# Performance work log

Hardware: AMD Instinct MI355X
Metric: run time of the kernel (lower is better)

Reference implementation:

```python
import jax, jax.numpy as jnp
import numpy as np

B, N, D, L = 32, 1024, 128, 2  # batch graphs, nodes, hidden dim, num GIN layers
BN_EPS = 1e-5


def _batchnorm(x2d, gamma, beta):
    # Training-mode BatchNorm1d over flattened (B*N, D) with biased variance
    mean = jnp.mean(x2d, axis=0)
    var = jnp.mean(jnp.square(x2d - mean), axis=0)
    return (x2d - mean) * (gamma / jnp.sqrt(var + BN_EPS)) + beta


def setup_inputs() -> dict:
    key = jax.random.key(0)
    ks = jax.random.split(key, 12)
    s = 1.0 / np.sqrt(D)  # torch Linear default init scale
    inp = {
        "x": jax.random.normal(ks[0], (B, N, D), dtype=jnp.float32),
        "padded_nei": jax.random.randint(ks[1], (B, N, 8), 0, N, dtype=jnp.int64),
        "adj": jax.random.uniform(ks[2], (B, N, N), dtype=jnp.float32),
        # stacked per-layer params [L, ...]
        "W1": jax.random.uniform(ks[3], (L, D, D), jnp.float32, -s, s),
        "b1": jax.random.uniform(ks[4], (L, D), jnp.float32, -s, s),
        "W2": jax.random.uniform(ks[5], (L, D, D), jnp.float32, -s, s),
        "b2": jax.random.uniform(ks[6], (L, D), jnp.float32, -s, s),
        "g_in": jnp.ones((L, D), jnp.float32),   # MLP-internal BN gamma
        "be_in": jnp.zeros((L, D), jnp.float32),  # MLP-internal BN beta
        "g_out": jnp.ones((L, D), jnp.float32),  # GraphCNN outer BN gamma
        "be_out": jnp.zeros((L, D), jnp.float32),
    }
    return inp


def reference(x, padded_nei, adj, W1, b1, W2, b2, g_in, be_in, g_out, be_out):
    h = x  # [B, N, D]
    for l in range(L):
        # sum-pooling over neighbors via batched dense adjacency matmul
        pooled = jnp.einsum('bij,bjd->bid', adj, h)  # [B, N, D]
        # MLP: Linear -> BN -> ReLU -> Linear
        z = pooled @ W1[l] + b1[l]
        z = jax.nn.relu(_batchnorm(z.reshape(-1, D), g_in[l], be_in[l])).reshape(B, N, D)
        z = z @ W2[l] + b2[l]
        # outer BatchNorm1d + ReLU
        h = jax.nn.relu(_batchnorm(z.reshape(-1, D), g_out[l], be_out[l])).reshape(B, N, D)
    return h
```

## Files before the change

### kernel.cpp

```cpp
#include <hip/hip_runtime.h>
#include <stdint.h>


#define BB 32
#define NN 1024
#define DD 128
#define RR 32768

typedef __bf16 bf16_t;
typedef bf16_t bf16x8 __attribute__((ext_vector_type(8)));
typedef float f32x4 __attribute__((ext_vector_type(4)));

__device__ __forceinline__ unsigned short f2b(float f) {
  unsigned u = __float_as_uint(f);
  u += 0x7fff + ((u >> 16) & 1);
  return (unsigned short)(u >> 16);
}
__device__ __forceinline__ float b2f(unsigned short s) {
  return __uint_as_float((unsigned)s << 16);
}

#define GLL(GP, LP)                                              \
  __builtin_amdgcn_global_load_lds(                              \
      (const __attribute__((address_space(1))) void*)(GP),       \
      (__attribute__((address_space(3))) void*)(LP), 16, 0, 0)

__global__ __launch_bounds__(256) void k0_prep(const float* __restrict__ x,
                                               const float* __restrict__ W1,
                                               const float* __restrict__ W2,
                                               unsigned short* __restrict__ hT,
                                               unsigned short* __restrict__ W1T,
                                               unsigned short* __restrict__ W2T) {
  const int tid = threadIdx.x;
  if (blockIdx.x < 256) {
    const int b = blockIdx.x >> 3, nt = blockIdx.x & 7;
    __shared__ alignas(16) unsigned short T[128][136];
    const int r = tid >> 1, c0 = (tid & 1) * 64;
    const float* src = x + ((size_t)(b * 8 + nt) * 128 + r) * 128 + c0;
#pragma unroll
    for (int i = 0; i < 64; i += 4) {
      float4 v = *(const float4*)(src + i);
      int c = c0 + i;
      T[c][r] = f2b(v.x); T[c + 1][r] = f2b(v.y);
      T[c + 2][r] = f2b(v.z); T[c + 3][r] = f2b(v.w);
    }
    __syncthreads();
    const int d = tid >> 1, n0 = (tid & 1) * 64;
    unsigned short* dst = hT + ((size_t)b * DD + d) * NN + nt * 128 + n0;
#pragma unroll
    for (int i = 0; i < 64; i += 8)
      *(uint4*)(dst + i) = *(const uint4*)&T[d][n0 + i];
  } else {
    int idx = (blockIdx.x - 256) * 256 + tid;
    int w = idx >> 15;
    int rem = idx & 32767;
    int l = rem >> 14;
    int n = (rem >> 7) & 127;
    int k = rem & 127;
    const float* W = w ? W2 : W1;
    unsigned short* WT = w ? W2T : W1T;
    WT[((size_t)l * 128 + n) * 128 + k] = f2b(W[((size_t)l * 128 + k) * 128 + n]);
  }
}

__global__ __launch_bounds__(256, 2) void kA_pool_lin(
    const float* __restrict__ adj, const unsigned short* __restrict__ hT,
    const unsigned short* __restrict__ WT, const float* __restrict__ bias,
    unsigned short* __restrict__ z1b, float* __restrict__ gsum,
    float* __restrict__ gsq) {
  const int mt = blockIdx.x, b = blockIdx.y;
  const int tid = threadIdx.x;
  const int wave = tid >> 6, lane = tid & 63;
  const int wc = wave * 32;
  const int ln = lane & 15, q = lane >> 4;

  __shared__ union {
    struct {
      float A[2][4096];
      unsigned short Bst[2][8192];
    } s;
    unsigned short As2[64][136];
  } sm;

  bf16x8 wfr[4][2];
#pragma unroll
  for (int ks = 0; ks < 4; ks++)
#pragma unroll
    for (int j = 0; j < 2; j++)
      wfr[ks][j] = *(const bf16x8*)&WT[(size_t)(wc + j * 16 + ln) * 128 + ks * 32 + q * 8];
  asm volatile("s_waitcnt vmcnt(0)" ::: "memory");

  const int rA = tid >> 4, uA = tid & 15;
  const float* gAf = adj + ((size_t)b * NN + mt * 64 + rA) * NN + ((uA ^ (rA & 7)) << 2);
  const int rB = tid >> 3, uB = tid & 7;
  const unsigned short* gBs =
      hT + (size_t)b * DD * NN + (size_t)rB * NN + ((uB ^ (rB & 7)) << 3);

#define STAGE(P, K0)                                \
  do {                                              \
    float* ap = sm.s.A[(P)];                        \
    unsigned short* bp = sm.s.Bst[(P)];             \
    GLL(gAf + (K0), ap + tid * 4);                  \
    GLL(gAf + 16 * NN + (K0), ap + 1024 + tid * 4); \
    GLL(gAf + 32 * NN + (K0), ap + 2048 + tid * 4); \
    GLL(gAf + 48 * NN + (K0), ap + 3072 + tid * 4); \
    GLL(gBs + (K0), bp + tid * 8);                  \
    GLL(gBs + 32 * NN + (K0), bp + 2048 + tid * 8); \
    GLL(gBs + 64 * NN + (K0), bp + 4096 + tid * 8); \
    GLL(gBs + 96 * NN + (K0), bp + 6144 + tid * 8); \
  } while (0)

  STAGE(0, 0);
  STAGE(1, 64);

  f32x4 acc1[4][2];
  f32x4 zero = {0.f, 0.f, 0.f, 0.f};
#pragma unroll
  for (int i = 0; i < 4; i++) { acc1[i][0] = zero; acc1[i][1] = zero; }

  const int x7 = ln & 7;
  const int xorvB = x7 << 4;

#pragma unroll 2
  for (int t = 0; t < 16; ++t) {
    const int p = t & 1;
    if (t < 15)
      asm volatile("s_waitcnt vmcnt(8)" ::: "memory");
    else
      asm volatile("s_waitcnt vmcnt(0)" ::: "memory");
    __builtin_amdgcn_s_barrier();
    __builtin_amdgcn_sched_barrier(0);
    {
      const float* Ab = sm.s.A[p];
      const char* Bb = (const char*)sm.s.Bst[p];
#pragma unroll
      for (int kk = 0; kk < 2; kk++) {
        const int cu = kk * 8 + q * 2;
        bf16x8 af[4], bfr[2];
#pragma unroll
        for (int i = 0; i < 4; i++) {
          const float* arow = Ab + (i * 16 + ln) * 64;
          float4 a0 = *(const float4*)(arow + ((cu ^ x7) << 2));
          float4 a1 = *(const float4*)(arow + (((cu + 1) ^ x7) << 2));
          bf16x8 v;
          v[0] = (bf16_t)a0.x; v[1] = (bf16_t)a0.y;
          v[2] = (bf16_t)a0.z; v[3] = (bf16_t)a0.w;
          v[4] = (bf16_t)a1.x; v[5] = (bf16_t)a1.y;
          v[6] = (bf16_t)a1.z; v[7] = (bf16_t)a1.w;
          af[i] = v;
        }
#pragma unroll
        for (int j = 0; j < 2; j++)
          bfr[j] = *(const bf16x8*)(Bb + (wc + j * 16 + ln) * 128 +
                                    (((kk << 6) + (q << 4)) ^ xorvB));
#pragma unroll
        for (int i = 0; i < 4; i++)
#pragma unroll
          for (int j = 0; j < 2; j++)
            acc1[i][j] = __builtin_amdgcn_mfma_f32_16x16x32_bf16(af[i], bfr[j], acc1[i][j], 0, 0, 0);
      }
    }
    __builtin_amdgcn_sched_barrier(0);
    __builtin_amdgcn_s_barrier();
    __builtin_amdgcn_sched_barrier(0);
    if (t < 14) STAGE(p, (t + 2) * 64);
  }
#undef STAGE

#pragma unroll
  for (int i = 0; i < 4; i++) {
    int row = i * 16 + q * 4;
#pragma unroll
    for (int j = 0; j < 2; j++) {
      int col = wc + j * 16 + ln;
#pragma unroll
      for (int r = 0; r < 4; r++) sm.As2[row + r][col] = f2b(acc1[i][j][r]);
    }
  }
  __syncthreads();

  f32x4 acc2[4][2];
#pragma unroll
  for (int i = 0; i < 4; i++) { acc2[i][0] = zero; acc2[i][1] = zero; }
#pragma unroll
  for (int ks = 0; ks < 4; ks++) {
    bf16x8 af[4];
#pragma unroll
    for (int i = 0; i < 4; i++)
      af[i] = *(const bf16x8*)&sm.As2[i * 16 + ln][ks * 32 + q * 8];
#pragma unroll
    for (int i = 0; i < 4; i++)
#pragma unroll
      for (int j = 0; j < 2; j++)
        acc2[i][j] = __builtin_amdgcn_mfma_f32_16x16x32_bf16(af[i], wfr[ks][j], acc2[i][j], 0, 0, 0);
  }

  const size_t row0 = (size_t)b * NN + mt * 64;
#pragma unroll
  for (int j = 0; j < 2; j++) {
    int col = wc + j * 16 + ln;
    float bc = bias[col];
    float s1 = 0.f, s2 = 0.f;
#pragma unroll
    for (int i = 0; i < 4; i++) {
      int row = i * 16 + q * 4;
#pragma unroll
      for (int r = 0; r < 4; r++) {
        float v = acc2[i][j][r] + bc;
        z1b[(row0 + row + r) * 128 + col] = f2b(v);
        s1 += v; s2 += v * v;
      }
    }
    s1 += __shfl_xor(s1, 16); s1 += __shfl_xor(s1, 32);
    s2 += __shfl_xor(s2, 16); s2 += __shfl_xor(s2, 32);
    if (q == 0) { atomicAdd(&gsum[col], s1); atomicAdd(&gsq[col], s2); }
  }
}

__global__ __launch_bounds__(256, 2) void kB_lin(
    const unsigned short* __restrict__ Zin, const float* __restrict__ gsum_in,
    const float* __restrict__ gsq_in, const float* __restrict__ gamma,
    const float* __restrict__ beta, const unsigned short* __restrict__ WT,
    const float* __restrict__ bias, unsigned short* __restrict__ z2b,
    float* __restrict__ gsum, float* __restrict__ gsq) {
  const int mt = blockIdx.x;
  const int tid = threadIdx.x;
  const int wave = tid >> 6, lane = tid & 63;
  const int wc = wave * 32;
  const int ln = lane & 15, q = lane >> 4;

  __shared__ alignas(16) unsigned short Az[64][136];
  __shared__ alignas(16) unsigned short Ws[128][136];
  __shared__ float nsc[128], nsh[128];

  if (tid < 128) {
    float mean = gsum_in[tid] * (1.f / 32768.f);
    float var = gsq_in[tid] * (1.f / 32768.f) - mean * mean;
    float sc = gamma[tid] * rsqrtf(var + 1e-5f);
    nsc[tid] = sc; nsh[tid] = beta[tid] - mean * sc;
  }
#pragma unroll
  for (int p = 0; p < 8; p++) {
    int c = tid + p * 256;
    int n = c >> 4, k8 = (c & 15) * 8;
    *(uint4*)&Ws[n][k8] = *(const uint4*)&WT[n * 128 + k8];
  }
  __syncthreads();

  const size_t row0 = (size_t)mt * 64;
  {
    const int r = tid >> 2, c0 = (tid & 3) * 32;
    const unsigned short* src = Zin + (row0 + r) * 128 + c0;
#pragma unroll
    for (int u = 0; u < 4; u++) {
      uint4 raw = *(const uint4*)(src + u * 8);
      const unsigned short* s = (const unsigned short*)&raw;
      alignas(16) unsigned short t[8];
#pragma unroll
      for (int e = 0; e < 8; e++) {
        int c = c0 + u * 8 + e;
        t[e] = f2b(fmaxf(fmaf(b2f(s[e]), nsc[c], nsh[c]), 0.f));
      }
      *(uint4*)&Az[r][c0 + u * 8] = *(const uint4*)&t[0];
    }
  }
  __syncthreads();

  f32x4 acc[4][2];
  f32x4 zero = {0.f, 0.f, 0.f, 0.f};
#pragma unroll
  for (int i = 0; i < 4; i++) { acc[i][0] = zero; acc[i][1] = zero; }
#pragma unroll
  for (int ks = 0; ks < 4; ks++) {
    bf16x8 af[4], bfr[2];
#pragma unroll
    for (int i = 0; i < 4; i++)
      af[i] = *(const bf16x8*)&Az[i * 16 + ln][ks * 32 + q * 8];
#pragma unroll
    for (int j = 0; j < 2; j++)
      bfr[j] = *(const bf16x8*)&Ws[wc + j * 16 + ln][ks * 32 + q * 8];
#pragma unroll
    for (int i = 0; i < 4; i++)
#pragma unroll
      for (int j = 0; j < 2; j++)
        acc[i][j] = __builtin_amdgcn_mfma_f32_16x16x32_bf16(af[i], bfr[j], acc[i][j], 0, 0, 0);
  }

#pragma unroll
  for (int j = 0; j < 2; j++) {
    int col = wc + j * 16 + ln;
    float bc = bias[col];
    float s1 = 0.f, s2 = 0.f;
#pragma unroll
    for (int i = 0; i < 4; i++) {
      int row = i * 16 + q * 4;
#pragma unroll
      for (int r = 0; r < 4; r++) {
        float v = acc[i][j][r] + bc;
        z2b[(row0 + row + r) * 128 + col] = f2b(v);
        s1 += v; s2 += v * v;
      }
    }
    s1 += __shfl_xor(s1, 16); s1 += __shfl_xor(s1, 32);
    s2 += __shfl_xor(s2, 16); s2 += __shfl_xor(s2, 32);
    if (q == 0) { atomicAdd(&gsum[col], s1); atomicAdd(&gsq[col], s2); }
  }
}

__global__ __launch_bounds__(256) void k4_bnt(const unsigned short* __restrict__ Z,
                                              const float* __restrict__ gsum,
                                              const float* __restrict__ gsq,
                                              const float* __restrict__ gamma,
                                              const float* __restrict__ beta,
                                              unsigned short* __restrict__ hT) {
  const int b = blockIdx.x, nt = blockIdx.y, tid = threadIdx.x;
  __shared__ alignas(16) unsigned short T[128][136];
  __shared__ float nsc[128], nsh[128];
  if (tid < 128) {
    float mean = gsum[tid] * (1.f / 32768.f);
    float var = gsq[tid] * (1.f / 32768.f) - mean * mean;
    float sc = gamma[tid] * rsqrtf(var + 1e-5f);
    nsc[tid] = sc; nsh[tid] = beta[tid] - mean * sc;
  }
  __syncthreads();
  const int r = tid >> 1, c0 = (tid & 1) * 64;
  const unsigned short* src = Z + ((size_t)(b * 8 + nt) * 128 + r) * 128 + c0;
#pragma unroll
  for (int u = 0; u < 8; u++) {
    uint4 raw = *(const uint4*)(src + u * 8);
    const unsigned short* s = (const unsigned short*)&raw;
#pragma unroll
    for (int e = 0; e < 8; e++) {
      int c = c0 + u * 8 + e;
      T[c][r] = f2b(fmaxf(fmaf(b2f(s[e]), nsc[c], nsh[c]), 0.f));
    }
  }
  __syncthreads();
  const int d = tid >> 1, n0 = (tid & 1) * 64;
  unsigned short* dst = hT + ((size_t)b * DD + d) * NN + nt * 128 + n0;
#pragma unroll
  for (int i = 0; i < 64; i += 8)
    *(uint4*)(dst + i) = *(const uint4*)&T[d][n0 + i];
}

__global__ __launch_bounds__(256) void k4_out(const unsigned short* __restrict__ Z,
                                              const float* __restrict__ gsum,
                                              const float* __restrict__ gsq,
                                              const float* __restrict__ gamma,
                                              const float* __restrict__ beta,
                                              float* __restrict__ out) {
  const int blk = blockIdx.x, tid = threadIdx.x;
  __shared__ float nsc[128], nsh[128];
  if (tid < 128) {
    float mean = gsum[tid] * (1.f / 32768.f);
    float var = gsq[tid] * (1.f / 32768.f) - mean * mean;
    float sc = gamma[tid] * rsqrtf(var + 1e-5f);
    nsc[tid] = sc; nsh[tid] = beta[tid] - mean * sc;
  }
  __syncthreads();
  const int r = tid >> 1, c0 = (tid & 1) * 64;
  const unsigned short* src = Z + ((size_t)blk * 128 + r) * 128 + c0;
  float* dst = out + ((size_t)blk * 128 + r) * 128 + c0;
#pragma unroll
  for (int u = 0; u < 8; u++) {
    uint4 raw = *(const uint4*)(src + u * 8);
    const unsigned short* s = (const unsigned short*)&raw;
    float4 o;
    int c = c0 + u * 8;
    o.x = fmaxf(fmaf(b2f(s[0]), nsc[c], nsh[c]), 0.f);
    o.y = fmaxf(fmaf(b2f(s[1]), nsc[c + 1], nsh[c + 1]), 0.f);
    o.z = fmaxf(fmaf(b2f(s[2]), nsc[c + 2], nsh[c + 2]), 0.f);
    o.w = fmaxf(fmaf(b2f(s[3]), nsc[c + 3], nsh[c + 3]), 0.f);
    *(float4*)(dst + u * 8) = o;
    o.x = fmaxf(fmaf(b2f(s[4]), nsc[c + 4], nsh[c + 4]), 0.f);
    o.y = fmaxf(fmaf(b2f(s[5]), nsc[c + 5], nsh[c + 5]), 0.f);
    o.z = fmaxf(fmaf(b2f(s[6]), nsc[c + 6], nsh[c + 6]), 0.f);
    o.w = fmaxf(fmaf(b2f(s[7]), nsc[c + 7], nsh[c + 7]), 0.f);
    *(float4*)(dst + u * 8 + 4) = o;
  }
}

extern "C" void kernel_launch(void* const* d_in, const int* in_sizes, int n_in,
                              void* d_out, int out_size, void* d_ws, size_t ws_size,
                              hipStream_t stream) {
  const float* x = (const float*)d_in[0];
  const float* adj = (const float*)d_in[2];
  const float* W1 = (const float*)d_in[3];
  const float* b1 = (const float*)d_in[4];
  const float* W2 = (const float*)d_in[5];
  const float* b2 = (const float*)d_in[6];
  const float* g_in = (const float*)d_in[7];
  const float* be_in = (const float*)d_in[8];
  const float* g_out = (const float*)d_in[9];
  const float* be_out = (const float*)d_in[10];
  float* out = (float*)d_out;

  char* ws = (char*)d_ws;
  unsigned short* hT = (unsigned short*)ws;
  unsigned short* z1b = (unsigned short*)(ws + 8ull * 1024 * 1024);
  unsigned short* z2b = (unsigned short*)(ws + 16ull * 1024 * 1024);
  unsigned short* W1T = (unsigned short*)(ws + 24ull * 1024 * 1024);
  unsigned short* W2T = W1T + 2 * 128 * 128;
  float* stats = (float*)(ws + 25ull * 1024 * 1024);

  hipMemsetAsync(stats, 0, 4 * 256 * sizeof(float), stream);
  k0_prep<<<512, 256, 0, stream>>>(x, W1, W2, hT, W1T, W2T);

  for (int l = 0; l < 2; l++) {
    float* st_in = stats + (l * 2 + 0) * 256;
    float* st_out = stats + (l * 2 + 1) * 256;
    kA_pool_lin<<<dim3(16, 32), 256, 0, stream>>>(adj, hT, W1T + l * 16384,
                                                  b1 + l * 128, z1b, st_in,
                                                  st_in + 128);
    kB_lin<<<512, 256, 0, stream>>>(z1b, st_in, st_in + 128, g_in + l * 128,
                                    be_in + l * 128, W2T + l * 16384,
                                    b2 + l * 128, z2b, st_out, st_out + 128);
    if (l == 0)
      k4_bnt<<<dim3(32, 8), 256, 0, stream>>>(z2b, st_out, st_out + 128, g_out,
                                              be_out, hT);
    else
      k4_out<<<256, 256, 0, stream>>>(z2b, st_out, st_out + 128, g_out + 128,
                                      be_out + 128, out);
  }
}
```

Before: 344.7 us.

## Fuse all stages into one persistent kernel with grid-wide barriers

Replaces the sequence of prep, pool+linear, linear, and BN-transpose/output launches with a single 512-block kernel that separates phases using a software grid barrier (atomic counter plus generation flag). The aim is to remove per-launch overhead and the idle tail between dependent kernels. It relies on all 512 blocks being co-resident (two per CU at 256 threads), and barrier spinning plus fences add their own latency. Shared memory becomes a union sized for the largest phase.

```diff
diff --git a/kernel.cpp b/kernel.cpp
--- a/kernel.cpp
+++ b/kernel.cpp
@@ -6,6 +6,7 @@
 #define NN 1024
 #define DD 128
 #define RR 32768
+#define NBLK 512
 
 typedef __bf16 bf16_t;
 typedef bf16_t bf16x8 __attribute__((ext_vector_type(8)));
@@ -25,33 +26,76 @@
       (const __attribute__((address_space(1))) void*)(GP),       \
       (__attribute__((address_space(3))) void*)(LP), 16, 0, 0)
 
-__global__ __launch_bounds__(256) void k0_prep(const float* __restrict__ x,
-                                               const float* __restrict__ W1,
-                                               const float* __restrict__ W2,
-                                               unsigned short* __restrict__ hT,
-                                               unsigned short* __restrict__ W1T,
-                                               unsigned short* __restrict__ W2T) {
+__device__ __forceinline__ void gsync(unsigned* bar) {
+  __syncthreads();
+  if (threadIdx.x == 0) {
+    __threadfence();
+    unsigned gen = __hip_atomic_load(bar + 1, __ATOMIC_RELAXED,
+                                     __HIP_MEMORY_SCOPE_AGENT);
+    unsigned prev = __hip_atomic_fetch_add(bar, 1u, __ATOMIC_ACQ_REL,
+                                           __HIP_MEMORY_SCOPE_AGENT);
+    if (prev == (unsigned)(NBLK - 1)) {
+      __hip_atomic_store(bar, 0u, __ATOMIC_RELAXED, __HIP_MEMORY_SCOPE_AGENT);
+      __hip_atomic_fetch_add(bar + 1, 1u, __ATOMIC_RELEASE,
+                             __HIP_MEMORY_SCOPE_AGENT);
+    } else {
+      while (__hip_atomic_load(bar + 1, __ATOMIC_RELAXED,
+                               __HIP_MEMORY_SCOPE_AGENT) == gen)
+        __builtin_amdgcn_s_sleep(2);
+    }
+    __threadfence();
+  }
+  __syncthreads();
+}
+
+__global__ __launch_bounds__(256, 2) void k_all(
+    const float* __restrict__ x, const float* __restrict__ adj,
+    const float* __restrict__ W1, const float* __restrict__ b1,
+    const float* __restrict__ W2, const float* __restrict__ b2,
+    const float* __restrict__ g_in, const float* __restrict__ be_in,
+    const float* __restrict__ g_out, const float* __restrict__ be_out,
+    float* __restrict__ out, unsigned short* __restrict__ hT,
+    unsigned short* __restrict__ z1b, unsigned short* __restrict__ z2b,
+    unsigned short* __restrict__ W1T, unsigned short* __restrict__ W2T,
+    float* __restrict__ stats, unsigned* __restrict__ bar) {
+  const int blk = blockIdx.x;
   const int tid = threadIdx.x;
-  if (blockIdx.x < 256) {
-    const int b = blockIdx.x >> 3, nt = blockIdx.x & 7;
-    __shared__ alignas(16) unsigned short T[128][136];
+
+  __shared__ union {
+    struct {
+      alignas(16) unsigned short T[128][136];
+    } t;
+    struct {
+      float A[2][4096];
+      unsigned short Bst[2][8192];
+    } a;
+    unsigned short As2[64][136];
+    struct {
+      alignas(16) unsigned short Az[64][136];
+      alignas(16) unsigned short Ws[128][136];
+    } b;
+  } sm;
+  __shared__ float nsc[128], nsh[128];
+
+  if (blk < 256) {
+    const int b = blk >> 3, nt = blk & 7;
     const int r = tid >> 1, c0 = (tid & 1) * 64;
     const float* src = x + ((size_t)(b * 8 + nt) * 128 + r) * 128 + c0;
 #pragma unroll
     for (int i = 0; i < 64; i += 4) {
       float4 v = *(const float4*)(src + i);
       int c = c0 + i;
-      T[c][r] = f2b(v.x); T[c + 1][r] = f2b(v.y);
-      T[c + 2][r] = f2b(v.z); T[c + 3][r] = f2b(v.w);
+      sm.t.T[c][r] = f2b(v.x); sm.t.T[c + 1][r] = f2b(v.y);
+      sm.t.T[c + 2][r] = f2b(v.z); sm.t.T[c + 3][r] = f2b(v.w);
     }
     __syncthreads();
     const int d = tid >> 1, n0 = (tid & 1) * 64;
     unsigned short* dst = hT + ((size_t)b * DD + d) * NN + nt * 128 + n0;
 #pragma unroll
     for (int i = 0; i < 64; i += 8)
-      *(uint4*)(dst + i) = *(const uint4*)&T[d][n0 + i];
+      *(uint4*)(dst + i) = *(const uint4*)&sm.t.T[d][n0 + i];
   } else {
-    int idx = (blockIdx.x - 256) * 256 + tid;
+    int idx = (blk - 256) * 256 + tid;
     int w = idx >> 15;
     int rem = idx & 32767;
     int l = rem >> 14;
@@ -61,322 +105,302 @@
     unsigned short* WT = w ? W2T : W1T;
     WT[((size_t)l * 128 + n) * 128 + k] = f2b(W[((size_t)l * 128 + k) * 128 + n]);
   }
-}
-
-__global__ __launch_bounds__(256, 2) void kA_pool_lin(
-    const float* __restrict__ adj, const unsigned short* __restrict__ hT,
-    const unsigned short* __restrict__ WT, const float* __restrict__ bias,
-    unsigned short* __restrict__ z1b, float* __restrict__ gsum,
-    float* __restrict__ gsq) {
-  const int mt = blockIdx.x, b = blockIdx.y;
-  const int tid = threadIdx.x;
-  const int wave = tid >> 6, lane = tid & 63;
-  const int wc = wave * 32;
-  const int ln = lane & 15, q = lane >> 4;
-
-  __shared__ union {
-    struct {
-      float A[2][4096];
-      unsigned short Bst[2][8192];
-    } s;
-    unsigned short As2[64][136];
-  } sm;
-
-  bf16x8 wfr[4][2];
-#pragma unroll
-  for (int ks = 0; ks < 4; ks++)
-#pragma unroll
-    for (int j = 0; j < 2; j++)
-      wfr[ks][j] = *(const bf16x8*)&WT[(size_t)(wc + j * 16 + ln) * 128 + ks * 32 + q * 8];
-  asm volatile("s_waitcnt vmcnt(0)" ::: "memory");
-
-  const int rA = tid >> 4, uA = tid & 15;
-  const float* gAf = adj + ((size_t)b * NN + mt * 64 + rA) * NN + ((uA ^ (rA & 7)) << 2);
-  const int rB = tid >> 3, uB = tid & 7;
-  const unsigned short* gBs =
-      hT + (size_t)b * DD * NN + (size_t)rB * NN + ((uB ^ (rB & 7)) << 3);
-
-#define STAGE(P, K0)                                \
-  do {                                              \
-    float* ap = sm.s.A[(P)];                        \
-    unsigned short* bp = sm.s.Bst[(P)];             \
-    GLL(gAf + (K0), ap + tid * 4);                  \
-    GLL(gAf + 16 * NN + (K0), ap + 1024 + tid * 4); \
-    GLL(gAf + 32 * NN + (K0), ap + 2048 + tid * 4); \
-    GLL(gAf + 48 * NN + (K0), ap + 3072 + tid * 4); \
-    GLL(gBs + (K0), bp + tid * 8);                  \
-    GLL(gBs + 32 * NN + (K0), bp + 2048 + tid * 8); \
-    GLL(gBs + 64 * NN + (K0), bp + 4096 + tid * 8); \
-    GLL(gBs + 96 * NN + (K0), bp + 6144 + tid * 8); \
+  gsync(bar);
+
+  for (int l = 0; l < 2; ++l) {
+    float* st_in = stats + (l * 2 + 0) * 256;
+    float* st_out = stats + (l * 2 + 1) * 256;
+
+    {
+      const int mt = blk & 15, b = blk >> 4;
+      const int wave = tid >> 6, lane = tid & 63;
+      const int wc = wave * 32;
+      const int ln = lane & 15, q = lane >> 4;
+      const unsigned short* WTa = W1T + l * 16384;
+      const float* biasA = b1 + l * 128;
+
+      bf16x8 wfr[4][2];
+#pragma unroll
+      for (int ks = 0; ks < 4; ks++)
+#pragma unroll
+        for (int j = 0; j < 2; j++)
+          wfr[ks][j] = *(const bf16x8*)&WTa[(size_t)(wc + j * 16 + ln) * 128 + ks * 32 + q * 8];
+      asm volatile("s_waitcnt vmcnt(0)" ::: "memory");
+
+      const int rA = tid >> 4, uA = tid & 15;
+      const float* gAf = adj + ((size_t)b * NN + mt * 64 + rA) * NN + ((uA ^ (rA & 7)) << 2);
+      const int rB = tid >> 3, uB = tid & 7;
+      const unsigned short* gBs =
+          hT + (size_t)b * DD * NN + (size_t)rB * NN + ((uB ^ (rB & 7)) << 3);
+
+#define STAGE(P, K0)                                  \
+  do {                                                \
+    float* ap = sm.a.A[(P)];                          \
+    unsigned short* bp = sm.a.Bst[(P)];               \
+    GLL(gAf + (K0), ap + tid * 4);                    \
+    GLL(gAf + 16 * NN + (K0), ap + 1024 + tid * 4);   \
+    GLL(gAf + 32 * NN + (K0), ap + 2048 + tid * 4);   \
+    GLL(gAf + 48 * NN + (K0), ap + 3072 + tid * 4);   \
+    GLL(gBs + (K0), bp + tid * 8);                    \
+    GLL(gBs + 32 * NN + (K0), bp + 2048 + tid * 8);   \
+    GLL(gBs + 64 * NN + (K0), bp + 4096 + tid * 8);   \
+    GLL(gBs + 96 * NN + (K0), bp + 6144 + tid * 8);   \
   } while (0)
 
-  STAGE(0, 0);
-  STAGE(1, 64);
-
-  f32x4 acc1[4][2];
-  f32x4 zero = {0.f, 0.f, 0.f, 0.f};
-#pragma unroll
-  for (int i = 0; i < 4; i++) { acc1[i][0] = zero; acc1[i][1] = zero; }
-
-  const int x7 = ln & 7;
-  const int xorvB = x7 << 4;
+      STAGE(0, 0);
+      STAGE(1, 64);
+
+      f32x4 acc1[4][2];
+      f32x4 zero = {0.f, 0.f, 0.f, 0.f};
+#pragma unroll
+      for (int i = 0; i < 4; i++) { acc1[i][0] = zero; acc1[i][1] = zero; }
+
+      const int x7 = ln & 7;
+      const int xorvB = x7 << 4;
 
 #pragma unroll 2
-  for (int t = 0; t < 16; ++t) {
-    const int p = t & 1;
-    if (t < 15)
-      asm volatile("s_waitcnt vmcnt(8)" ::: "memory");
-    else
-      asm volatile("s_waitcnt vmcnt(0)" ::: "memory");
-    __builtin_amdgcn_s_barrier();
-    __builtin_amdgcn_sched_barrier(0);
+      for (int t = 0; t < 16; ++t) {
+        const int p = t & 1;
+        if (t < 15)
+          asm volatile("s_waitcnt vmcnt(8)" ::: "memory");
+        else
+          asm volatile("s_waitcnt vmcnt(0)" ::: "memory");
+        __builtin_amdgcn_s_barrier();
+        __builtin_amdgcn_sched_barrier(0);
+        {
+          const float* Ab = sm.a.A[p];
+          const char* Bb = (const char*)sm.a.Bst[p];
+#pragma unroll
+          for (int kk = 0; kk < 2; kk++) {
+            const int cu = kk * 8 + q * 2;
+            bf16x8 af[4], bfr[2];
+#pragma unroll
+            for (int i = 0; i < 4; i++) {
+              const float* arow = Ab + (i * 16 + ln) * 64;
+              float4 a0 = *(const float4*)(arow + ((cu ^ x7) << 2));
+              float4 a1 = *(const float4*)(arow + (((cu + 1) ^ x7) << 2));
+              bf16x8 v;
+              v[0] = (bf16_t)a0.x; v[1] = (bf16_t)a0.y;
+              v[2] = (bf16_t)a0.z; v[3] = (bf16_t)a0.w;
+              v[4] = (bf16_t)a1.x; v[5] = (bf16_t)a1.y;
+              v[6] = (bf16_t)a1.z; v[7] = (bf16_t)a1.w;
+              af[i] = v;
+            }
+#pragma unroll
+            for (int j = 0; j < 2; j++)
+              bfr[j] = *(const bf16x8*)(Bb + (wc + j * 16 + ln) * 128 +
+                                        (((kk << 6) + (q << 4)) ^ xorvB));
+#pragma unroll
+            for (int i = 0; i < 4; i++)
+#pragma unroll
+              for (int j = 0; j < 2; j++)
+                acc1[i][j] = __builtin_amdgcn_mfma_f32_16x16x32_bf16(af[i], bfr[j], acc1[i][j], 0, 0, 0);
+          }
+        }
+        __builtin_amdgcn_sched_barrier(0);
+        __builtin_amdgcn_s_barrier();
+        __builtin_amdgcn_sched_barrier(0);
+        if (t < 14) STAGE(p, (t + 2) * 64);
+      }
+#undef STAGE
+
+#pragma unroll
+      for (int i = 0; i < 4; i++) {
+        int row = i * 16 + q * 4;
+#pragma unroll
+        for (int j = 0; j < 2; j++) {
+          int col = wc + j * 16 + ln;
+#pragma unroll
+          for (int r = 0; r < 4; r++) sm.As2[row + r][col] = f2b(acc1[i][j][r]);
+        }
+      }
+      __syncthreads();
+
+      f32x4 acc2[4][2];
+#pragma unroll
+      for (int i = 0; i < 4; i++) { acc2[i][0] = zero; acc2[i][1] = zero; }
+#pragma unroll
+      for (int ks = 0; ks < 4; ks++) {
+        bf16x8 af[4];
+#pragma unroll
+        for (int i = 0; i < 4; i++)
+          af[i] = *(const bf16x8*)&sm.As2[i * 16 + ln][ks * 32 + q * 8];
+#pragma unroll
+        for (int i = 0; i < 4; i++)
+#pragma unroll
+          for (int j = 0; j < 2; j++)
+            acc2[i][j] = __builtin_amdgcn_mfma_f32_16x16x32_bf16(af[i], wfr[ks][j], acc2[i][j], 0, 0, 0);
+      }
+
+      const size_t row0 = (size_t)b * NN + mt * 64;
+#pragma unroll
+      for (int j = 0; j < 2; j++) {
+        int col = wc + j * 16 + ln;
+        float bc = biasA[col];
+        float s1 = 0.f, s2 = 0.f;
+#pragma unroll
+        for (int i = 0; i < 4; i++) {
+          int row = i * 16 + q * 4;
+#pragma unroll
+          for (int r = 0; r < 4; r++) {
+            float v = acc2[i][j][r] + bc;
+            z1b[(row0 + row + r) * 128 + col] = f2b(v);
+            s1 += v; s2 += v * v;
+          }
+        }
+        s1 += __shfl_xor(s1, 16); s1 += __shfl_xor(s1, 32);
+        s2 += __shfl_xor(s2, 16); s2 += __shfl_xor(s2, 32);
+        if (q == 0) { atomicAdd(&st_in[col], s1); atomicAdd(&st_in[128 + col], s2); }
+      }
+    }
+    gsync(bar);
+
     {
-      const float* Ab = sm.s.A[p];
-      const char* Bb = (const char*)sm.s.Bst[p];
-#pragma unroll
-      for (int kk = 0; kk < 2; kk++) {
-        const int cu = kk * 8 + q * 2;
+      const int mt = blk;
+      const int wave = tid >> 6, lane = tid & 63;
+      const int wc = wave * 32;
+      const int ln = lane & 15, q = lane >> 4;
+      const unsigned short* WTb = W2T + l * 16384;
+      const float* biasB = b2 + l * 128;
+      const float* gam = g_in + l * 128;
+      const float* bet = be_in + l * 128;
+
+      if (tid < 128) {
+        float mean = st_in[tid] * (1.f / 32768.f);
+        float var = st_in[128 + tid] * (1.f / 32768.f) - mean * mean;
+        float sc = gam[tid] * rsqrtf(var + 1e-5f);
+        nsc[tid] = sc; nsh[tid] = bet[tid] - mean * sc;
+      }
+#pragma unroll
+      for (int p = 0; p < 8; p++) {
+        int c = tid + p * 256;
+        int n = c >> 4, k8 = (c & 15) * 8;
+        *(uint4*)&sm.b.Ws[n][k8] = *(const uint4*)&WTb[n * 128 + k8];
+      }
+      __syncthreads();
+
+      const size_t row0 = (size_t)mt * 64;
+      {
+        const int r = tid >> 2, c0 = (tid & 3) * 32;
+        const unsigned short* src = z1b + (row0 + r) * 128 + c0;
+#pragma unroll
+        for (int u = 0; u < 4; u++) {
+          uint4 raw = *(const uint4*)(src + u * 8);
+          const unsigned short* s = (const unsigned short*)&raw;
+          alignas(16) unsigned short tmp[8];
+#pragma unroll
+          for (int e = 0; e < 8; e++) {
+            int c = c0 + u * 8 + e;
+            tmp[e] = f2b(fmaxf(fmaf(b2f(s[e]), nsc[c], nsh[c]), 0.f));
+          }
+          *(uint4*)&sm.b.Az[r][c0 + u * 8] = *(const uint4*)&tmp[0];
+        }
+      }
+      __syncthreads();
+
+      f32x4 acc[4][2];
+      f32x4 zero = {0.f, 0.f, 0.f, 0.f};
+#pragma unroll
+      for (int i = 0; i < 4; i++) { acc[i][0] = zero; acc[i][1] = zero; }
+#pragma unroll
+      for (int ks = 0; ks < 4; ks++) {
         bf16x8 af[4], bfr[2];
 #pragma unroll
+        for (int i = 0; i < 4; i++)
+          af[i] = *(const bf16x8*)&sm.b.Az[i * 16 + ln][ks * 32 + q * 8];
+#pragma unroll
+        for (int j = 0; j < 2; j++)
+          bfr[j] = *(const bf16x8*)&sm.b.Ws[wc + j * 16 + ln][ks * 32 + q * 8];
+#pragma unroll
+        for (int i = 0; i < 4; i++)
+#pragma unroll
+          for (int j = 0; j < 2; j++)
+            acc[i][j] = __builtin_amdgcn_mfma_f32_16x16x32_bf16(af[i], bfr[j], acc[i][j], 0, 0, 0);
+      }
+
+#pragma unroll
+      for (int j = 0; j < 2; j++) {
+        int col = wc + j * 16 + ln;
+        float bc = biasB[col];
+        float s1 = 0.f, s2 = 0.f;
+#pragma unroll
         for (int i = 0; i < 4; i++) {
-          const float* arow = Ab + (i * 16 + ln) * 64;
-          float4 a0 = *(const float4*)(arow + ((cu ^ x7) << 2));
-          float4 a1 = *(const float4*)(arow + (((cu + 1) ^ x7) << 2));
-          bf16x8 v;
-          v[0] = (bf16_t)a0.x; v[1] = (bf16_t)a0.y;
-          v[2] = (bf16_t)a0.z; v[3] = (bf16_t)a0.w;
-          v[4] = (bf16_t)a1.x; v[5] = (bf16_t)a1.y;
-          v[6] = (bf16_t)a1.z; v[7] = (bf16_t)a1.w;
-          af[i] = v;
-        }
-#pragma unroll
-        for (int j = 0; j < 2; j++)
-          bfr[j] = *(const bf16x8*)(Bb + (wc + j * 16 + ln) * 128 +
-                                    (((kk << 6) + (q << 4)) ^ xorvB));
-#pragma unroll
-        for (int i = 0; i < 4; i++)
-#pragma unroll
-          for (int j = 0; j < 2; j++)
-            acc1[i][j] = __builtin_amdgcn_mfma_f32_16x16x32_bf16(af[i], bfr[j], acc1[i][j], 0, 0, 0);
+          int row = i * 16 + q * 4;
+#pragma unroll
+          for (int r = 0; r < 4; r++) {
+            float v = acc[i][j][r] + bc;
+            z2b[(row0 + row + r) * 128 + col] = f2b(v);
+            s1 += v; s2 += v * v;
+          }
+        }
+        s1 += __shfl_xor(s1, 16); s1 += __shfl_xor(s1, 32);
+        s2 += __shfl_xor(s2, 16); s2 += __shfl_xor(s2, 32);
+        if (q == 0) { atomicAdd(&st_out[col], s1); atomicAdd(&st_out[128 + col], s2); }
       }
     }
-    __builtin_amdgcn_sched_barrier(0);
-    __builtin_amdgcn_s_barrier();
-    __builtin_amdgcn_sched_barrier(0);
-    if (t < 14) STAGE(p, (t + 2) * 64);
-  }
-#undef STAGE
-
-#pragma unroll
-  for (int i = 0; i < 4; i++) {
-    int row = i * 16 + q * 4;
-#pragma unroll
-    for (int j = 0; j < 2; j++) {
-      int col = wc + j * 16 + ln;
-#pragma unroll
-      for (int r = 0; r < 4; r++) sm.As2[row + r][col] = f2b(acc1[i][j][r]);
+    gsync(bar);
+
+    if (l == 0) {
+      const int b = blk >> 4, nseg = blk & 15;
+      if (tid < 128) {
+        float mean = st_out[tid] * (1.f / 32768.f);
+        float var = st_out[128 + tid] * (1.f / 32768.f) - mean * mean;
+        float sc = g_out[tid] * rsqrtf(var + 1e-5f);
+        nsc[tid] = sc; nsh[tid] = be_out[tid] - mean * sc;
+      }
+      __syncthreads();
+      const size_t zrow0 = (size_t)b * NN + nseg * 64;
+      {
+        const int r = tid >> 2, c0 = (tid & 3) * 32;
+        const unsigned short* src = z2b + (zrow0 + r) * 128 + c0;
+#pragma unroll
+        for (int u = 0; u < 4; u++) {
+          uint4 raw = *(const uint4*)(src + u * 8);
+          const unsigned short* s = (const unsigned short*)&raw;
+#pragma unroll
+          for (int e = 0; e < 8; e++) {
+            int c = c0 + u * 8 + e;
+            sm.t.T[c][r] = f2b(fmaxf(fmaf(b2f(s[e]), nsc[c], nsh[c]), 0.f));
+          }
+        }
+      }
+      __syncthreads();
+      const int d = tid >> 1, nh = (tid & 1) * 32;
+      unsigned short* dst = hT + ((size_t)b * DD + d) * NN + nseg * 64 + nh;
+#pragma unroll
+      for (int i = 0; i < 32; i += 8)
+        *(uint4*)(dst + i) = *(const uint4*)&sm.t.T[d][nh + i];
+      gsync(bar);
+    } else {
+      if (tid < 128) {
+        float mean = st_out[tid] * (1.f / 32768.f);
+        float var = st_out[128 + tid] * (1.f / 32768.f) - mean * mean;
+        float sc = g_out[128 + tid] * rsqrtf(var + 1e-5f);
+        nsc[tid] = sc; nsh[tid] = be_out[128 + tid] - mean * sc;
+      }
+      __syncthreads();
+      const size_t row0 = (size_t)blk * 64;
+      const int r = tid >> 2, c0 = (tid & 3) * 32;
+      const unsigned short* src = z2b + (row0 + r) * 128 + c0;
+      float* dst = out + (row0 + r) * 128 + c0;
+#pragma unroll
+      for (int u = 0; u < 4; u++) {
+        uint4 raw = *(const uint4*)(src + u * 8);
+        const unsigned short* s = (const unsigned short*)&raw;
+        float4 o;
+        int c = c0 + u * 8;
+        o.x = fmaxf(fmaf(b2f(s[0]), nsc[c], nsh[c]), 0.f);
+        o.y = fmaxf(fmaf(b2f(s[1]), nsc[c + 1], nsh[c + 1]), 0.f);
+        o.z = fmaxf(fmaf(b2f(s[2]), nsc[c + 2], nsh[c + 2]), 0.f);
+        o.w = fmaxf(fmaf(b2f(s[3]), nsc[c + 3], nsh[c + 3]), 0.f);
+        *(float4*)(dst + u * 8) = o;
+        o.x = fmaxf(fmaf(b2f(s[4]), nsc[c + 4], nsh[c + 4]), 0.f);
+        o.y = fmaxf(fmaf(b2f(s[5]), nsc[c + 5], nsh[c + 5]), 0.f);
+        o.z = fmaxf(fmaf(b2f(s[6]), nsc[c + 6], nsh[c + 6]), 0.f);
+        o.w = fmaxf(fmaf(b2f(s[7]), nsc[c + 7], nsh[c + 7]), 0.f);
+        *(float4*)(dst + u * 8 + 4) = o;
+      }
     }
-  }
-  __syncthreads();
-
-  f32x4 acc2[4][2];
-#pragma unroll
-  for (int i = 0; i < 4; i++) { acc2[i][0] = zero; acc2[i][1] = zero; }
-#pragma unroll
-  for (int ks = 0; ks < 4; ks++) {
-    bf16x8 af[4];
-#pragma unroll
-    for (int i = 0; i < 4; i++)
-      af[i] = *(const bf16x8*)&sm.As2[i * 16 + ln][ks * 32 + q * 8];
-#pragma unroll
-    for (int i = 0; i < 4; i++)
-#pragma unroll
-      for (int j = 0; j < 2; j++)
-        acc2[i][j] = __builtin_amdgcn_mfma_f32_16x16x32_bf16(af[i], wfr[ks][j], acc2[i][j], 0, 0, 0);
-  }
-
-  const size_t row0 = (size_t)b * NN + mt * 64;
-#pragma unroll
-  for (int j = 0; j < 2; j++) {
-    int col = wc + j * 16 + ln;
-    float bc = bias[col];
-    float s1 = 0.f, s2 = 0.f;
-#pragma unroll
-    for (int i = 0; i < 4; i++) {
-      int row = i * 16 + q * 4;
-#pragma unroll
-      for (int r = 0; r < 4; r++) {
-        float v = acc2[i][j][r] + bc;
-        z1b[(row0 + row + r) * 128 + col] = f2b(v);
-        s1 += v; s2 += v * v;
-      }
-    }
-    s1 += __shfl_xor(s1, 16); s1 += __shfl_xor(s1, 32);
-    s2 += __shfl_xor(s2, 16); s2 += __shfl_xor(s2, 32);
-    if (q == 0) { atomicAdd(&gsum[col], s1); atomicAdd(&gsq[col], s2); }
-  }
-}
-
-__global__ __launch_bounds__(256, 2) void kB_lin(
-    const unsigned short* __restrict__ Zin, const float* __restrict__ gsum_in,
-    const float* __restrict__ gsq_in, const float* __restrict__ gamma,
-    const float* __restrict__ beta, const unsigned short* __restrict__ WT,
-    const float* __restrict__ bias, unsigned short* __restrict__ z2b,
-    float* __restrict__ gsum, float* __restrict__ gsq) {
-  const int mt = blockIdx.x;
-  const int tid = threadIdx.x;
-  const int wave = tid >> 6, lane = tid & 63;
-  const int wc = wave * 32;
-  const int ln = lane & 15, q = lane >> 4;
-
-  __shared__ alignas(16) unsigned short Az[64][136];
-  __shared__ alignas(16) unsigned short Ws[128][136];
-  __shared__ float nsc[128], nsh[128];
-
-  if (tid < 128) {
-    float mean = gsum_in[tid] * (1.f / 32768.f);
-    float var = gsq_in[tid] * (1.f / 32768.f) - mean * mean;
-    float sc = gamma[tid] * rsqrtf(var + 1e-5f);
-    nsc[tid] = sc; nsh[tid] = beta[tid] - mean * sc;
-  }
-#pragma unroll
-  for (int p = 0; p < 8; p++) {
-    int c = tid + p * 256;
-    int n = c >> 4, k8 = (c & 15) * 8;
-    *(uint4*)&Ws[n][k8] = *(const uint4*)&WT[n * 128 + k8];
-  }
-  __syncthreads();
-
-  const size_t row0 = (size_t)mt * 64;
-  {
-    const int r = tid >> 2, c0 = (tid & 3) * 32;
-    const unsigned short* src = Zin + (row0 + r) * 128 + c0;
-#pragma unroll
-    for (int u = 0; u < 4; u++) {
-      uint4 raw = *(const uint4*)(src + u * 8);
-      const unsigned short* s = (const unsigned short*)&raw;
-      alignas(16) unsigned short t[8];
-#pragma unroll
-      for (int e = 0; e < 8; e++) {
-        int c = c0 + u * 8 + e;
-        t[e] = f2b(fmaxf(fmaf(b2f(s[e]), nsc[c], nsh[c]), 0.f));
-      }
-      *(uint4*)&Az[r][c0 + u * 8] = *(const uint4*)&t[0];
-    }
-  }
-  __syncthreads();
-
-  f32x4 acc[4][2];
-  f32x4 zero = {0.f, 0.f, 0.f, 0.f};
-#pragma unroll
-  for (int i = 0; i < 4; i++) { acc[i][0] = zero; acc[i][1] = zero; }
-#pragma unroll
-  for (int ks = 0; ks < 4; ks++) {
-    bf16x8 af[4], bfr[2];
-#pragma unroll
-    for (int i = 0; i < 4; i++)
-      af[i] = *(const bf16x8*)&Az[i * 16 + ln][ks * 32 + q * 8];
-#pragma unroll
-    for (int j = 0; j < 2; j++)
-      bfr[j] = *(const bf16x8*)&Ws[wc + j * 16 + ln][ks * 32 + q * 8];
-#pragma unroll
-    for (int i = 0; i < 4; i++)
-#pragma unroll
-      for (int j = 0; j < 2; j++)
-        acc[i][j] = __builtin_amdgcn_mfma_f32_16x16x32_bf16(af[i], bfr[j], acc[i][j], 0, 0, 0);
-  }
-
-#pragma unroll
-  for (int j = 0; j < 2; j++) {
-    int col = wc + j * 16 + ln;
-    float bc = bias[col];
-    float s1 = 0.f, s2 = 0.f;
-#pragma unroll
-    for (int i = 0; i < 4; i++) {
-      int row = i * 16 + q * 4;
-#pragma unroll
-      for (int r = 0; r < 4; r++) {
-        float v = acc[i][j][r] + bc;
-        z2b[(row0 + row + r) * 128 + col] = f2b(v);
-        s1 += v; s2 += v * v;
-      }
-    }
-    s1 += __shfl_xor(s1, 16); s1 += __shfl_xor(s1, 32);
-    s2 += __shfl_xor(s2, 16); s2 += __shfl_xor(s2, 32);
-    if (q == 0) { atomicAdd(&gsum[col], s1); atomicAdd(&gsq[col], s2); }
-  }
-}
-
-__global__ __launch_bounds__(256) void k4_bnt(const unsigned short* __restrict__ Z,
-                                              const float* __restrict__ gsum,
-                                              const float* __restrict__ gsq,
-                                              const float* __restrict__ gamma,
-                                              const float* __restrict__ beta,
-                                              unsigned short* __restrict__ hT) {
-  const int b = blockIdx.x, nt = blockIdx.y, tid = threadIdx.x;
-  __shared__ alignas(16) unsigned short T[128][136];
-  __shared__ float nsc[128], nsh[128];
-  if (tid < 128) {
-    float mean = gsum[tid] * (1.f / 32768.f);
-    float var = gsq[tid] * (1.f / 32768.f) - mean * mean;
-    float sc = gamma[tid] * rsqrtf(var + 1e-5f);
-    nsc[tid] = sc; nsh[tid] = beta[tid] - mean * sc;
-  }
-  __syncthreads();
-  const int r = tid >> 1, c0 = (tid & 1) * 64;
-  const unsigned short* src = Z + ((size_t)(b * 8 + nt) * 128 + r) * 128 + c0;
-#pragma unroll
-  for (int u = 0; u < 8; u++) {
-    uint4 raw = *(const uint4*)(src + u * 8);
-    const unsigned short* s = (const unsigned short*)&raw;
-#pragma unroll
-    for (int e = 0; e < 8; e++) {
-      int c = c0 + u * 8 + e;
-      T[c][r] = f2b(fmaxf(fmaf(b2f(s[e]), nsc[c], nsh[c]), 0.f));
-    }
-  }
-  __syncthreads();
-  const int d = tid >> 1, n0 = (tid & 1) * 64;
-  unsigned short* dst = hT + ((size_t)b * DD + d) * NN + nt * 128 + n0;
-#pragma unroll
-  for (int i = 0; i < 64; i += 8)
-    *(uint4*)(dst + i) = *(const uint4*)&T[d][n0 + i];
-}
-
-__global__ __launch_bounds__(256) void k4_out(const unsigned short* __restrict__ Z,
-                                              const float* __restrict__ gsum,
-                                              const float* __restrict__ gsq,
-                                              const float* __restrict__ gamma,
-                                              const float* __restrict__ beta,
-                                              float* __restrict__ out) {
-  const int blk = blockIdx.x, tid = threadIdx.x;
-  __shared__ float nsc[128], nsh[128];
-  if (tid < 128) {
-    float mean = gsum[tid] * (1.f / 32768.f);
-    float var = gsq[tid] * (1.f / 32768.f) - mean * mean;
-    float sc = gamma[tid] * rsqrtf(var + 1e-5f);
-    nsc[tid] = sc; nsh[tid] = beta[tid] - mean * sc;
-  }
-  __syncthreads();
-  const int r = tid >> 1, c0 = (tid & 1) * 64;
-  const unsigned short* src = Z + ((size_t)blk * 128 + r) * 128 + c0;
-  float* dst = out + ((size_t)blk * 128 + r) * 128 + c0;
-#pragma unroll
-  for (int u = 0; u < 8; u++) {
-    uint4 raw = *(const uint4*)(src + u * 8);
-    const unsigned short* s = (const unsigned short*)&raw;
-    float4 o;
-    int c = c0 + u * 8;
-    o.x = fmaxf(fmaf(b2f(s[0]), nsc[c], nsh[c]), 0.f);
-    o.y = fmaxf(fmaf(b2f(s[1]), nsc[c + 1], nsh[c + 1]), 0.f);
-    o.z = fmaxf(fmaf(b2f(s[2]), nsc[c + 2], nsh[c + 2]), 0.f);
-    o.w = fmaxf(fmaf(b2f(s[3]), nsc[c + 3], nsh[c + 3]), 0.f);
-    *(float4*)(dst + u * 8) = o;
-    o.x = fmaxf(fmaf(b2f(s[4]), nsc[c + 4], nsh[c + 4]), 0.f);
-    o.y = fmaxf(fmaf(b2f(s[5]), nsc[c + 5], nsh[c + 5]), 0.f);
-    o.z = fmaxf(fmaf(b2f(s[6]), nsc[c + 6], nsh[c + 6]), 0.f);
-    o.w = fmaxf(fmaf(b2f(s[7]), nsc[c + 7], nsh[c + 7]), 0.f);
-    *(float4*)(dst + u * 8 + 4) = o;
   }
 }
 
@@ -402,24 +426,10 @@
   unsigned short* W1T = (unsigned short*)(ws + 24ull * 1024 * 1024);
   unsigned short* W2T = W1T + 2 * 128 * 128;
   float* stats = (float*)(ws + 25ull * 1024 * 1024);
-
-  hipMemsetAsync(stats, 0, 4 * 256 * sizeof(float), stream);
-  k0_prep<<<512, 256, 0, stream>>>(x, W1, W2, hT, W1T, W2T);
-
-  for (int l = 0; l < 2; l++) {
-    float* st_in = stats + (l * 2 + 0) * 256;
-    float* st_out = stats + (l * 2 + 1) * 256;
-    kA_pool_lin<<<dim3(16, 32), 256, 0, stream>>>(adj, hT, W1T + l * 16384,
-                                                  b1 + l * 128, z1b, st_in,
-                                                  st_in + 128);
-    kB_lin<<<512, 256, 0, stream>>>(z1b, st_in, st_in + 128, g_in + l * 128,
-                                    be_in + l * 128, W2T + l * 16384,
-                                    b2 + l * 128, z2b, st_out, st_out + 128);
-    if (l == 0)
-      k4_bnt<<<dim3(32, 8), 256, 0, stream>>>(z2b, st_out, st_out + 128, g_out,
-                                              be_out, hT);
-    else
-      k4_out<<<256, 256, 0, stream>>>(z2b, st_out, st_out + 128, g_out + 128,
-                                      be_out + 128, out);
-  }
+  unsigned* bar = (unsigned*)(stats + 4 * 256);
+
+  hipMemsetAsync(stats, 0, 4 * 256 * sizeof(float) + 64, stream);
+  k_all<<<NBLK, 256, 0, stream>>>(x, adj, W1, b1, W2, b2, g_in, be_in, g_out,
+                                  be_out, out, hT, z1b, z2b, W1T, W2T, stats,
+                                  bar);
 }
```

Result: slower. 801.9 us (+132.6%).
